# Kernel optimization log

Hardware: AMD Instinct MI355X
Metric: run time of the kernel (lower is better)

## Reference

```python
import jax, jax.numpy as jnp
import numpy as np

SR = 44100
PRE_EMPH = 0.97
FRAME_LEN = int(0.02 * SR)      # 882
FRAME_HOP = FRAME_LEN // 2      # 441
N_FFT = 2048
EPS = 1e-10


def setup_inputs() -> dict:
    key = jax.random.key(0)
    k1, k2 = jax.random.split(key)
    waveform = jax.random.normal(k1, (16, 441000), dtype=jnp.float32)
    # librosa mel filterbank is a fixed nonnegative (n_mels, n_fft//2+1) matrix;
    # a random surrogate keeps the math (dense matmul) identical.
    mel_filters = jax.random.uniform(k2, (60, N_FFT // 2 + 1), dtype=jnp.float32)
    return {"waveform": waveform, "mel_filters": mel_filters}


def _mfdwc(waveform, mel_filters):
    dt = waveform.dtype
    # pre-emphasis: y[0]=x[0], y[t]=x[t]-0.97*x[t-1]
    emph = jnp.concatenate(
        [waveform[:, :1], waveform[:, 1:] - PRE_EMPH * waveform[:, :-1]], axis=1)
    L = emph.shape[1]
    n_frames = 1 + (L - FRAME_LEN) // FRAME_HOP  # static
    idx = jnp.arange(n_frames)[:, None] * FRAME_HOP + jnp.arange(FRAME_LEN)[None, :]
    frames = emph[:, idx]                                   # (B, T, 882)
    window = jnp.asarray(np.hamming(FRAME_LEN), dtype=dt)   # (882,)
    windowed = frames * window
    spec = jnp.fft.rfft(windowed, n=N_FFT, axis=-1)         # (B, T, 1025) complex
    power = jnp.real(spec) ** 2 + jnp.imag(spec) ** 2       # |FFT|^2
    mel = jnp.einsum('mf,btf->btm', mel_filters, power)     # (B, T, 60)
    logmel = jnp.log(mel + EPS)
    # 1-level Haar DWT along mel axis (pywt convention, even length):
    # cA = (x_even + x_odd)/sqrt(2), cD = (x_even - x_odd)/sqrt(2)
    sq2 = jnp.sqrt(jnp.asarray(2.0, dt))
    x_even, x_odd = logmel[..., 0::2], logmel[..., 1::2]
    cA = (x_even + x_odd) / sq2                             # (B, T, 30)
    cD = (x_even - x_odd) / sq2                             # (B, T, 30)
    # delta (window=3, edge-padded): d[t] = a[clamp(t+1)] - a[clamp(t-1)]
    fwd = jnp.concatenate([cA[:, 1:], cA[:, -1:]], axis=1)
    bwd = jnp.concatenate([cA[:, :1], cA[:, :-1]], axis=1)
    delta = fwd - bwd
    feats = jnp.concatenate([cA, delta, cD], axis=-1)       # (B, T, 90)
    mean = jnp.mean(feats, axis=1)
    std = jnp.std(feats, axis=1, ddof=1)                    # torch.std unbiased
    return jnp.concatenate([mean, std], axis=1)             # (B, 180)


def reference(waveform, mel_filters):
    return _mfdwc(waveform, mel_filters)
```

## Files before the change

kernel.cpp:

```cpp
#include <hip/hip_runtime.h>
#include <hip/hip_bf16.h>
#include <math.h>

#define FRAME_LEN 882
#define FRAME_HOP 441
#define NFFT 2048
#define NFRAMES 999
#define NBATCH 16
#define NMEL 60
#define WAVE_LEN 441000
#define PRE_EMPH 0.97f
#define EPS 1e-10f
#define NROWS (NBATCH * NFRAMES)
#define NPANEL 999
#define KPAD 1056
#define NKC 33
#define PANEL_ELEMS (NKC * 512)
#define PANEL_BYTES (PANEL_ELEMS * 2)
#define PI_F 3.14159265358979323846f

#define PADI(i) ((i) + ((i) >> 4))

__device__ __forceinline__ int frag_off(int m, int k) {
  return ((k >> 5) * 512) | (((k >> 3) & 3) * 128) | (m * 8) | (k & 7);
}

typedef float vf2 __attribute__((ext_vector_type(2)));
__device__ __forceinline__ vf2 mkv(float x, float y){ vf2 r; r.x = x; r.y = y; return r; }
__device__ __forceinline__ vf2 cmul(vf2 a, vf2 b){ return a.xx * b + mkv(-a.y, a.y) * b.yx; }
__device__ __forceinline__ vf2 rotni(vf2 z){ return mkv(z.y, -z.x); }

__device__ __forceinline__ void dif_group16(vf2* x, vf2 t1, bool zerohi) {
  const vf2 C81 = mkv(0.9238795325f, -0.3826834324f);
  const vf2 C82 = mkv(0.7071067812f, -0.7071067812f);
  const vf2 C83 = mkv(0.3826834324f, -0.9238795325f);
  vf2 w0 = t1, w1 = cmul(t1, C81), w2 = cmul(t1, C82), w3 = cmul(t1, C83);
  vf2 ws1[8] = {w0, w1, w2, w3, rotni(w0), rotni(w1), rotni(w2), rotni(w3)};
  if (zerohi) {
#pragma unroll
    for (int k = 0; k < 8; ++k) x[k + 8] = cmul(x[k], ws1[k]);
  } else {
#pragma unroll
    for (int k = 0; k < 8; ++k) {
      vf2 u = x[k], v = x[k + 8];
      x[k] = u + v;
      x[k + 8] = cmul(u - v, ws1[k]);
    }
  }
  vf2 t2 = cmul(t1, t1);
  vf2 v1 = cmul(t2, C82);
  vf2 ws2[4] = {t2, v1, rotni(t2), rotni(v1)};
#pragma unroll
  for (int h = 0; h < 2; ++h) {
#pragma unroll
    for (int k = 0; k < 4; ++k) {
      vf2 u = x[h*8 + k], v = x[h*8 + k + 4];
      x[h*8 + k] = u + v;
      x[h*8 + k + 4] = cmul(u - v, ws2[k]);
    }
  }
  vf2 t4 = cmul(t2, t2);
  vf2 t4r = rotni(t4);
#pragma unroll
  for (int h = 0; h < 4; ++h) {
    vf2 a = x[h*4 + 0], b = x[h*4 + 2];
    x[h*4 + 0] = a + b; x[h*4 + 2] = cmul(a - b, t4);
    a = x[h*4 + 1]; b = x[h*4 + 3];
    x[h*4 + 1] = a + b; x[h*4 + 3] = cmul(a - b, t4r);
  }
  vf2 t8 = cmul(t4, t4);
#pragma unroll
  for (int j = 0; j < 8; ++j) {
    vf2 a = x[2*j], b = x[2*j + 1];
    x[2*j] = a + b; x[2*j + 1] = cmul(a - b, t8);
  }
}

__device__ __forceinline__ void dif8(vf2* y) {
  const vf2 c1 = mkv(0.7071067812f, -0.7071067812f);
  const vf2 c3 = mkv(-0.7071067812f, -0.7071067812f);
  vf2 u, v;
  u=y[0]; v=y[4]; y[0]=u+v; y[4]=u-v;
  u=y[1]; v=y[5]; y[1]=u+v; y[5]=cmul(u-v, c1);
  u=y[2]; v=y[6]; y[2]=u+v; y[6]=rotni(u-v);
  u=y[3]; v=y[7]; y[3]=u+v; y[7]=cmul(u-v, c3);
  u=y[0]; v=y[2]; y[0]=u+v; y[2]=u-v;
  u=y[1]; v=y[3]; y[1]=u+v; y[3]=rotni(u-v);
  u=y[4]; v=y[6]; y[4]=u+v; y[6]=u-v;
  u=y[5]; v=y[7]; y[5]=u+v; y[7]=rotni(u-v);
  u=y[0]; v=y[1]; y[0]=u+v; y[1]=u-v;
  u=y[2]; v=y[3]; y[2]=u+v; y[3]=u-v;
  u=y[4]; v=y[5]; y[4]=u+v; y[5]=u-v;
  u=y[6]; v=y[7]; y[6]=u+v; y[7]=u-v;
}

__global__ __launch_bounds__(256) void fft_pow_kernel(
    const float* __restrict__ wav, const float* __restrict__ filt,
    __hip_bfloat16* __restrict__ powrF, __hip_bfloat16* __restrict__ filtbF)
{
  __shared__ vf2 lds2[2][NFFT + (NFFT >> 4)];
  const int id = blockIdx.x;

  if (id >= 4000) {
    const int mm = id - 4000;
    __hip_bfloat16* qp = filtbF + (size_t)(mm >> 4) * PANEL_ELEMS;
    const int m = mm & 15;
    for (int k = threadIdx.x; k < KPAD; k += 256) {
      float v = (mm < NMEL && k < 1025) ? filt[mm * 1025 + k] : 0.f;
      qp[frag_off(m, k)] = __float2bfloat16(v);
    }
    return;
  }

  const int t   = threadIdx.x;
  const int fid = t >> 7;
  const int tt  = t & 127;
  vf2* lds = lds2[fid];

  const int P  = id * 2 + fid;
  const int b  = P & 15;
  const int t0 = 2 * (P >> 4), t1f = t0 + 1;
  const bool has1 = (t1f < NFRAMES);
  const float* w = wav + (size_t)b * WAVE_LEN;
  const int s0 = t0 * FRAME_HOP;
  int s1 = t1f * FRAME_HOP;
  if (s1 > WAVE_LEN - FRAME_LEN) s1 = WAVE_LEN - FRAME_LEN;

  vf2 x[16];
  {
    float sB, cB, sD, cD;
    __sincosf(6.283185307179586f * (float)tt / 881.0f, &sB, &cB);
    __sincosf(6.283185307179586f * 128.0f / 881.0f, &sD, &cD);
    vf2 cur  = mkv(cB, sB);
    vf2 step = mkv(cD, sD);
#pragma unroll
    for (int k = 0; k < 7; ++k) {
      int i = k * 128 + tt;
      float v1 = 0.f, v2 = 0.f;
      if (i < FRAME_LEN) {
        float win = 0.54f - 0.46f * cur.x;
        int s = s0 + i;
        float e1 = (s > 0) ? (w[s] - PRE_EMPH * w[s - 1]) : w[s];
        v1 = e1 * win;
        int ss = s1 + i;
        v2 = (w[ss] - PRE_EMPH * w[ss - 1]) * win;
      }
      x[k] = mkv(v1, v2);
      cur = cmul(cur, step);
    }
#pragma unroll
    for (int k = 7; k < 16; ++k) x[k] = mkv(0.f, 0.f);
  }

  {
    float sA, cA;
    __sincosf(-PI_F * (float)tt / 1024.0f, &sA, &cA);
    dif_group16(x, mkv(cA, sA), true);
  }
#pragma unroll
  for (int k = 0; k < 16; ++k) lds[PADI(k * 128 + tt)] = x[k];
  __syncthreads();

  {
    const int Q = tt >> 3, r = tt & 7;
    const int base = Q * 128 + r;
#pragma unroll
    for (int k = 0; k < 16; ++k) x[k] = lds[PADI(base + k * 8)];
    float sA, cA;
    __sincosf(-PI_F * (float)r / 64.0f, &sA, &cA);
    dif_group16(x, mkv(cA, sA), false);
#pragma unroll
    for (int k = 0; k < 16; ++k) lds[PADI(base + k * 8)] = x[k];
  }
  __syncthreads();

  {
    vf2 ya[8], yb[8];
#pragma unroll
    for (int j = 0; j < 8; ++j) {
      ya[j] = lds[PADI(16 * tt + j)];
      yb[j] = lds[PADI(16 * tt + 8 + j)];
    }
    dif8(ya);
    dif8(yb);
    __syncthreads();
    const int r7 = (int)(__brev((unsigned)tt) >> 25);
    const int RA[8] = {0, 8, 4, 12, 2, 10, 6, 14};
    const int RB[8] = {1, 9, 5, 13, 3, 11, 7, 15};
#pragma unroll
    for (int j = 0; j < 8; ++j) {
      lds[PADI(RA[j] * 128 + r7)] = ya[j];
      lds[PADI(RB[j] * 128 + r7)] = yb[j];
    }
  }
  __syncthreads();

  const int r0g = b * NFRAMES + t0;
  const int r1g = r0g + 1;
  __hip_bfloat16* q0 = powrF + (size_t)(r0g >> 4) * PANEL_ELEMS;
  const int m0 = r0g & 15;
  __hip_bfloat16* q1 = powrF + (size_t)(r1g >> 4) * PANEL_ELEMS;
  const int m1 = r1g & 15;
#pragma unroll
  for (int c = 0; c < 8; ++c) {
    int f = c * 128 + tt;
    int mir = (NFFT - f) & (NFFT - 1);
    vf2 z = lds[PADI(f)];
    vf2 y = lds[PADI(mir)];
    float f1r = z.x + y.x, f1i = z.y - y.y;
    float f2r = z.y + y.y, f2i = y.x - z.x;
    float pw1 = 0.25f * (f1r * f1r + f1i * f1i);
    float pw2 = 0.25f * (f2r * f2r + f2i * f2i);
    q0[frag_off(m0, f)] = __float2bfloat16(pw1);
    if (has1) q1[frag_off(m1, f)] = __float2bfloat16(pw2);
  }
  if (tt == 0) {
    vf2 z = lds[PADI(1024)];
    q0[frag_off(m0, 1024)] = __float2bfloat16(z.x * z.x);
    if (has1) q1[frag_off(m1, 1024)] = __float2bfloat16(z.y * z.y);
  }
  if (tt < KPAD - 1025) {
    int f = 1025 + tt;
    q0[frag_off(m0, f)] = __float2bfloat16(0.f);
    if (has1) q1[frag_off(m1, f)] = __float2bfloat16(0.f);
  }
}

typedef __attribute__((ext_vector_type(8))) short short8x;
typedef __attribute__((ext_vector_type(4))) float float4x;

__global__ __launch_bounds__(256) void melgemm_kernel(
    const __hip_bfloat16* __restrict__ powrF,
    const __hip_bfloat16* __restrict__ filtbF,
    float* __restrict__ logmelT)
{
  __shared__ __hip_bfloat16 As[PANEL_ELEMS];
  const int tid  = threadIdx.x;
  const int wave = tid >> 6, lane = tid & 63;
  const int p = blockIdx.x;
  const __hip_bfloat16* pA = powrF + (size_t)p * PANEL_ELEMS;

#pragma unroll
  for (int r = 0; r < 9; ++r) {
    const int off = r * 4096 + tid * 16;
    if (off < PANEL_BYTES) {
      __builtin_amdgcn_global_load_lds(
          (const __attribute__((address_space(1))) unsigned int*)
              ((const unsigned char*)pA + off),
          (__attribute__((address_space(3))) unsigned int*)
              ((unsigned char*)As + off),
          16, 0, 0);
    }
  }
  __syncthreads();

  const __hip_bfloat16* pB = filtbF + (size_t)wave * PANEL_ELEMS + lane * 8;

  float4x acc0 = {0.f, 0.f, 0.f, 0.f};
  float4x acc1 = {0.f, 0.f, 0.f, 0.f};
#pragma unroll 4
  for (int kc = 0; kc < 16; ++kc) {
    short8x b0 = *(const short8x*)(pB + kc * 512);
    short8x b1 = *(const short8x*)(pB + (kc + 16) * 512);
    short8x a0 = *(const short8x*)(&As[kc * 512 + lane * 8]);
    short8x a1 = *(const short8x*)(&As[(kc + 16) * 512 + lane * 8]);
    acc0 = __builtin_amdgcn_mfma_f32_16x16x32_bf16(a0, b0, acc0, 0, 0, 0);
    acc1 = __builtin_amdgcn_mfma_f32_16x16x32_bf16(a1, b1, acc1, 0, 0, 0);
  }
  {
    short8x bf = *(const short8x*)(pB + 32 * 512);
    short8x a  = *(const short8x*)(&As[32 * 512 + lane * 8]);
    acc0 = __builtin_amdgcn_mfma_f32_16x16x32_bf16(a, bf, acc0, 0, 0, 0);
  }

  const int mel = wave * 16 + (lane & 15);
  const int rsub = (lane >> 4) * 4;
  if (mel < NMEL) {
#pragma unroll
    for (int reg = 0; reg < 4; ++reg) {
      int row = p * 16 + rsub + reg;
      float vv = acc0[reg] + acc1[reg];
      logmelT[(size_t)mel * NROWS + row] = __logf(vv + EPS);
    }
  }
}

__global__ __launch_bounds__(256) void stats_kernel(
    const float* __restrict__ lmT, float* __restrict__ out)
{
  __shared__ float red[4];
  const int j   = blockIdx.x;
  const int b   = blockIdx.y;
  const int tid = threadIdx.x;
  const int base = b * NFRAMES;
  const float inv_sq2 = 0.7071067811865475f;
  const bool v3 = (tid < NFRAMES - 768);

  float f0, f1, f2, f3;
  if (j < 30) {
    const float* e = lmT + (size_t)(2 * j) * NROWS + base;
    const float* o = lmT + (size_t)(2 * j + 1) * NROWS + base;
    f0 = (e[tid]       + o[tid])       * inv_sq2;
    f1 = (e[tid + 256] + o[tid + 256]) * inv_sq2;
    f2 = (e[tid + 512] + o[tid + 512]) * inv_sq2;
    f3 = v3 ? (e[tid + 768] + o[tid + 768]) * inv_sq2 : 0.f;
  } else if (j < 60) {
    const int m = j - 30;
    const float* e = lmT + (size_t)(2 * m) * NROWS + base;
    const float* o = lmT + (size_t)(2 * m + 1) * NROWS + base;
    auto dl = [&](int t) -> float {
      int tp = (t + 1 > NFRAMES - 1) ? (NFRAMES - 1) : (t + 1);
      int tm = (t - 1 < 0) ? 0 : (t - 1);
      return ((e[tp] + o[tp]) - (e[tm] + o[tm])) * inv_sq2;
    };
    f0 = dl(tid);
    f1 = dl(tid + 256);
    f2 = dl(tid + 512);
    f3 = v3 ? dl(tid + 768) : 0.f;
  } else {
    const int m = j - 60;
    const float* e = lmT + (size_t)(2 * m) * NROWS + base;
    const float* o = lmT + (size_t)(2 * m + 1) * NROWS + base;
    f0 = (e[tid]       - o[tid])       * inv_sq2;
    f1 = (e[tid + 256] - o[tid + 256]) * inv_sq2;
    f2 = (e[tid + 512] - o[tid + 512]) * inv_sq2;
    f3 = v3 ? (e[tid + 768] - o[tid + 768]) * inv_sq2 : 0.f;
  }

  float s = f0 + f1 + f2 + f3;
  for (int o2 = 32; o2 > 0; o2 >>= 1) s += __shfl_xor(s, o2, 64);
  if ((tid & 63) == 0) red[tid >> 6] = s;
  __syncthreads();
  float mean = (red[0] + red[1] + red[2] + red[3]) / (float)NFRAMES;
  __syncthreads();

  float d0 = f0 - mean, d1 = f1 - mean, d2 = f2 - mean;
  float d3 = v3 ? (f3 - mean) : 0.f;
  float s2 = d0 * d0 + d1 * d1 + d2 * d2 + d3 * d3;
  for (int o2 = 32; o2 > 0; o2 >>= 1) s2 += __shfl_xor(s2, o2, 64);
  if ((tid & 63) == 0) red[tid >> 6] = s2;
  __syncthreads();
  float var = (red[0] + red[1] + red[2] + red[3]) / (float)(NFRAMES - 1);

  if (tid == 0) {
    out[b * 180 + j]      = mean;
    out[b * 180 + 90 + j] = sqrtf(var);
  }
}

extern "C" void kernel_launch(void* const* d_in, const int* in_sizes, int n_in,
                              void* d_out, int out_size, void* d_ws, size_t ws_size,
                              hipStream_t stream) {
  const float* wav  = (const float*)d_in[0];
  const float* filt = (const float*)d_in[1];
  float* out = (float*)d_out;

  unsigned char* ws = (unsigned char*)d_ws;
  __hip_bfloat16* powrF  = (__hip_bfloat16*)(ws);
  size_t off = (size_t)NPANEL * PANEL_ELEMS * 2;
  __hip_bfloat16* filtbF = (__hip_bfloat16*)(ws + off);
  off += (size_t)4 * PANEL_ELEMS * 2;
  float* logmelT = (float*)(ws + off);

  fft_pow_kernel<<<4064, 256, 0, stream>>>(wav, filt, powrF, filtbF);
  melgemm_kernel<<<NPANEL, 256, 0, stream>>>(powrF, filtbF, logmelT);
  stats_kernel<<<dim3(90, NBATCH), 256, 0, stream>>>(logmelT, out);
}
```

Before: 113.7 us.

## Process two panels per block with register-resident B and double-buffered LDS

The mel GEMM kernel now handles two row panels per block. Each lane loads all 33 filter fragments into registers once, and the next panel's LDS copy is issued while the current one is computed, alternating between two LDS buffers. The aim is to cut repeated global loads of the filterbank and hide panel load latency behind MFMA work. In exchange, register pressure rises sharply (33 short8 vectors per lane) and the grid drops to 500 blocks, which lowers parallelism and occupancy.

```diff
diff --git a/kernel.cpp b/kernel.cpp
--- a/kernel.cpp
+++ b/kernel.cpp
@@ -229,59 +229,78 @@
 typedef __attribute__((ext_vector_type(8))) short short8x;
 typedef __attribute__((ext_vector_type(4))) float float4x;
 
+#define PPB 2
+
 __global__ __launch_bounds__(256) void melgemm_kernel(
     const __hip_bfloat16* __restrict__ powrF,
     const __hip_bfloat16* __restrict__ filtbF,
     float* __restrict__ logmelT)
 {
-  __shared__ __hip_bfloat16 As[PANEL_ELEMS];
+  __shared__ __hip_bfloat16 As[2][PANEL_ELEMS];
   const int tid  = threadIdx.x;
   const int wave = tid >> 6, lane = tid & 63;
-  const int p = blockIdx.x;
-  const __hip_bfloat16* pA = powrF + (size_t)p * PANEL_ELEMS;
-
-#pragma unroll
-  for (int r = 0; r < 9; ++r) {
-    const int off = r * 4096 + tid * 16;
-    if (off < PANEL_BYTES) {
-      __builtin_amdgcn_global_load_lds(
-          (const __attribute__((address_space(1))) unsigned int*)
-              ((const unsigned char*)pA + off),
-          (__attribute__((address_space(3))) unsigned int*)
-              ((unsigned char*)As + off),
-          16, 0, 0);
-    }
-  }
-  __syncthreads();
-
-  const __hip_bfloat16* pB = filtbF + (size_t)wave * PANEL_ELEMS + lane * 8;
-
-  float4x acc0 = {0.f, 0.f, 0.f, 0.f};
-  float4x acc1 = {0.f, 0.f, 0.f, 0.f};
-#pragma unroll 4
-  for (int kc = 0; kc < 16; ++kc) {
-    short8x b0 = *(const short8x*)(pB + kc * 512);
-    short8x b1 = *(const short8x*)(pB + (kc + 16) * 512);
-    short8x a0 = *(const short8x*)(&As[kc * 512 + lane * 8]);
-    short8x a1 = *(const short8x*)(&As[(kc + 16) * 512 + lane * 8]);
-    acc0 = __builtin_amdgcn_mfma_f32_16x16x32_bf16(a0, b0, acc0, 0, 0, 0);
-    acc1 = __builtin_amdgcn_mfma_f32_16x16x32_bf16(a1, b1, acc1, 0, 0, 0);
-  }
-  {
-    short8x bf = *(const short8x*)(pB + 32 * 512);
-    short8x a  = *(const short8x*)(&As[32 * 512 + lane * 8]);
-    acc0 = __builtin_amdgcn_mfma_f32_16x16x32_bf16(a, bf, acc0, 0, 0, 0);
-  }
-
-  const int mel = wave * 16 + (lane & 15);
+  const int p0 = blockIdx.x * PPB;
+
+  short8x Breg[NKC];
+  {
+    const __hip_bfloat16* pB = filtbF + (size_t)wave * PANEL_ELEMS + lane * 8;
+#pragma unroll
+    for (int kc = 0; kc < NKC; ++kc)
+      Breg[kc] = *(const short8x*)(pB + kc * 512);
+  }
+
+  auto stage = [&](int buf, int p) {
+    const unsigned char* src =
+        (const unsigned char*)(powrF + (size_t)p * PANEL_ELEMS);
+    unsigned char* dst = (unsigned char*)As[buf];
+#pragma unroll
+    for (int r = 0; r < 9; ++r) {
+      const int off = r * 4096 + tid * 16;
+      if (off < PANEL_BYTES) {
+        __builtin_amdgcn_global_load_lds(
+            (const __attribute__((address_space(1))) unsigned int*)(src + off),
+            (__attribute__((address_space(3))) unsigned int*)(dst + off),
+            16, 0, 0);
+      }
+    }
+  };
+
+  stage(0, p0);
+  __syncthreads();
+
+  const int mel  = wave * 16 + (lane & 15);
   const int rsub = (lane >> 4) * 4;
-  if (mel < NMEL) {
-#pragma unroll
-    for (int reg = 0; reg < 4; ++reg) {
-      int row = p * 16 + rsub + reg;
-      float vv = acc0[reg] + acc1[reg];
-      logmelT[(size_t)mel * NROWS + row] = __logf(vv + EPS);
-    }
+
+  for (int i = 0; i < PPB; ++i) {
+    const int p = p0 + i;
+    if (p >= NPANEL) break;
+    const bool more = (i + 1 < PPB) && (p + 1 < NPANEL);
+    if (more) stage((i + 1) & 1, p + 1);
+
+    const __hip_bfloat16* A = As[i & 1];
+    float4x acc0 = {0.f, 0.f, 0.f, 0.f};
+    float4x acc1 = {0.f, 0.f, 0.f, 0.f};
+#pragma unroll
+    for (int kc = 0; kc < 16; ++kc) {
+      short8x a0 = *(const short8x*)(&A[kc * 512 + lane * 8]);
+      short8x a1 = *(const short8x*)(&A[(kc + 16) * 512 + lane * 8]);
+      acc0 = __builtin_amdgcn_mfma_f32_16x16x32_bf16(a0, Breg[kc], acc0, 0, 0, 0);
+      acc1 = __builtin_amdgcn_mfma_f32_16x16x32_bf16(a1, Breg[kc + 16], acc1, 0, 0, 0);
+    }
+    {
+      short8x a = *(const short8x*)(&A[32 * 512 + lane * 8]);
+      acc0 = __builtin_amdgcn_mfma_f32_16x16x32_bf16(a, Breg[32], acc0, 0, 0, 0);
+    }
+
+    if (mel < NMEL) {
+#pragma unroll
+      for (int reg = 0; reg < 4; ++reg) {
+        int row = p * 16 + rsub + reg;
+        float vv = acc0[reg] + acc1[reg];
+        logmelT[(size_t)mel * NROWS + row] = __logf(vv + EPS);
+      }
+    }
+    if (more) __syncthreads();
   }
 }
 
@@ -363,6 +382,6 @@
   float* logmelT = (float*)(ws + off);
 
   fft_pow_kernel<<<4064, 256, 0, stream>>>(wav, filt, powrF, filtbF);
-  melgemm_kernel<<<NPANEL, 256, 0, stream>>>(powrF, filtbF, logmelT);
+  melgemm_kernel<<<500, 256, 0, stream>>>(powrF, filtbF, logmelT);
   stats_kernel<<<dim3(90, NBATCH), 256, 0, stream>>>(logmelT, out);
 }
```

After: 112.9 us. About the same (-0.7%).
